# Performance work log

Hardware: AMD Instinct MI355X
Metric: run time of the kernel (lower is better)

## Reference

```python
import jax, jax.numpy as jnp
import numpy as np
from jax.ops import segment_sum, segment_max

N, D, B = 1536, 32, 8            # nodes, candidate out-degree per node, sequential batch steps
OBS, HID, HEADS, C = 33, 64, 4, 8  # obs_dim, GRU hidden, attn heads, out_dim//heads
E = N * D


def setup_inputs() -> dict:
    key = jax.random.key(0)
    ks = jax.random.split(key, 16)
    g = lambda i, shape, s=0.1: jax.random.normal(ks[i], shape, jnp.float32) * s
    src = jnp.repeat(jnp.arange(N), D)                    # uniform degree -> scatter_topk = row top-k
    dst = jax.random.randint(ks[0], (E,), 0, N)
    return dict(
        H_t=jax.random.normal(ks[1], (B, N, OBS), jnp.float32),
        src=src, dst=dst, k=4,
        W_e1=g(2, (OBS, 32)), b_e1=jnp.zeros(32), W_e2=g(3, (32, 32)), b_e2=jnp.zeros(32),
        ln_g=jnp.ones(32), ln_b=jnp.zeros(32),
        W_ih=g(4, (3 * HID, 32)), W_hh=g(5, (3 * HID, HID)),
        b_ih=jnp.zeros(3 * HID), b_hh=jnp.zeros(3 * HID),
        W_s1=g(6, (2 * HID, 64)), b_s1=jnp.zeros(64), W_s2=g(7, (64, 1)), b_s2=jnp.zeros(1),
        W_gat=g(8, (HID, HEADS * C)), att_src=g(9, (HEADS, C)), att_dst=g(10, (HEADS, C)),
        b_gat=jnp.zeros(HEADS * C),
    )


def _layernorm(x, g, b, eps=1e-5):
    mu = x.mean(-1, keepdims=True)
    var = ((x - mu) ** 2).mean(-1, keepdims=True)
    return (x - mu) * jax.lax.rsqrt(var + eps) * g + b


def _forward(H_t, src, dst, k, W_e1, b_e1, W_e2, b_e2, ln_g, ln_b,
             W_ih, W_hh, b_ih, b_hh, W_s1, b_s1, W_s2, b_s2,
             W_gat, att_src, att_dst, b_gat):
    # ObsEmbedding: Linear-ReLU-Linear-ReLU-LayerNorm, applied to all (B,N) at once
    x = jax.nn.relu(H_t @ W_e1 + b_e1)
    x = jax.nn.relu(x @ W_e2 + b_e2)
    H_emb = _layernorm(x, ln_g, ln_b)              # (B,N,32)

    def step(h, e_t):
        # --- NodeMemory: shared GRUCell, h carried across batch steps ---
        gi = e_t @ W_ih.T + b_ih                   # (N,3H)
        gh = h @ W_hh.T + b_hh
        i_r, i_z, i_n = jnp.split(gi, 3, -1)
        h_r, h_z, h_n = jnp.split(gh, 3, -1)
        r = jax.nn.sigmoid(i_r + h_r)
        z = jax.nn.sigmoid(i_z + h_z)
        n = jnp.tanh(i_n + r * h_n)
        h_new = (1.0 - z) * n + z * h              # (N,HID)

        # --- EdgeScorer: sigmoid MLP score per candidate edge, keep top-k per source ---
        feat = jnp.concatenate([h_new[src], h_new[dst]], -1)        # (E,2*HID)
        score = jax.nn.sigmoid(
            (jax.nn.relu(feat @ W_s1 + b_s1) @ W_s2 + b_s2)[:, 0])  # (E,)
        s2 = score.reshape(N, D)
        top_idx = jax.lax.top_k(s2, k)[1]                           # (N,k)
        keep = (jnp.zeros((N, D), bool)
                .at[jnp.arange(N)[:, None], top_idx].set(True)).reshape(-1)  # (E,)
        w = jnp.where(keep, score, 0.0)                             # soft edge weights

        # --- GATConv (add_self_loops=False), pruned edges masked out of the softmax ---
        xh = (h_new @ W_gat).reshape(N, HEADS, C)
        a_s = (xh * att_src).sum(-1)               # (N,HEADS)
        a_d = (xh * att_dst).sum(-1)
        logit = jax.nn.leaky_relu(a_s[src] + a_d[dst], 0.2)         # (E,HEADS)
        logit = jnp.where(keep[:, None], logit, -1e30)
        m = segment_max(logit, dst, num_segments=N)                 # softmax grouped by target
        ex = jnp.where(keep[:, None], jnp.exp(logit - m[dst]), 0.0)
        ssum = segment_sum(ex, dst, num_segments=N)
        alpha = ex / jnp.clip(ssum[dst], 1e-16)                     # (E,HEADS)

        msg = alpha[:, :, None] * xh[src] * w[:, None, None]        # edge_weight scales messages
        out = segment_sum(msg, dst, num_segments=N).reshape(N, HEADS * C) + b_gat

        # --- densify attention: scatter-accumulate then row-normalize ---
        A = jnp.zeros((HEADS, N, N), alpha.dtype).at[:, src, dst].add(alpha.T)
        A = A / jnp.clip(A.sum(-1, keepdims=True), 1e-9)
        return h_new, (out, A)

    h0 = jnp.zeros((N, HID), H_t.dtype)
    _, (outs, attns) = jax.lax.scan(step, h0, H_emb)
    return outs, attns                              # (B,N,32), (B,HEADS,N,N)


def reference(H_t, src, dst, k, W_e1, b_e1, W_e2, b_e2, ln_g, ln_b,
              W_ih, W_hh, b_ih, b_hh, W_s1, b_s1, W_s2, b_s2,
              W_gat, att_src, att_dst, b_gat):
    return _forward(H_t, src, dst, k, W_e1, b_e1, W_e2, b_e2, ln_g, ln_b,
                    W_ih, W_hh, b_ih, b_hh, W_s1, b_s1, W_s2, b_s2,
                    W_gat, att_src, att_dst, b_gat)
```

## Files before the change

### kernel.cpp

```cpp
#include <hip/hip_runtime.h>
#include <math.h>

#define NN   1536
#define DG   32
#define BB   8
#define OBSD 33
#define HID  64
#define NHEAD 4
#define EE   (NN*DG)

__device__ __forceinline__ float sigm(float x){ return 1.0f/(1.0f+expf(-x)); }

__global__ void __launch_bounds__(256) k_embgi(
                      const float* __restrict__ Ht,
                      const float* __restrict__ We1, const float* __restrict__ be1,
                      const float* __restrict__ We2, const float* __restrict__ be2,
                      const float* __restrict__ lng, const float* __restrict__ lnb,
                      const float* __restrict__ Wih, const float* __restrict__ bih,
                      float* __restrict__ GI, int* __restrict__ cursor){
    __shared__ float lwih[192*33];
    int tid = threadIdx.x;
    if(blockIdx.x < 6) cursor[blockIdx.x*256 + tid] = 0;
    for(int i=tid;i<192*32;i+=256){ int r=i>>5, c=i&31; lwih[r*33+c]=Wih[i]; }
    __syncthreads();
    int lane = tid & 63;
    int j32 = lane & 31;
    int bn = blockIdx.x*4 + (tid>>6);
    const float* hrow = Ht + (size_t)bn*OBSD;
    float x1 = be1[j32];
    for(int o=0;o<OBSD;o++) x1 += hrow[o]*We1[o*32+j32];
    x1 = fmaxf(x1,0.f);
    float x2 = be2[j32];
    for(int i=0;i<32;i++){
        float xi = __shfl(x1, (lane & 32) | i, 64);
        x2 += xi * We2[i*32+j32];
    }
    x2 = fmaxf(x2,0.f);
    float mu = x2;
    for(int m=16;m>=1;m>>=1) mu += __shfl_xor(mu, m, 32);
    mu *= (1.0f/32.0f);
    float d = x2-mu; float var = d*d;
    for(int m=16;m>=1;m>>=1) var += __shfl_xor(var, m, 32);
    var *= (1.0f/32.0f);
    float xln = d*rsqrtf(var+1e-5f)*lng[j32]+lnb[j32];
    int j = lane;
    float gr=bih[j], gz=bih[64+j], gn=bih[128+j];
    for(int kk=0;kk<32;kk++){
        float ek = __shfl(xln, kk, 64);
        gr += ek*lwih[j*33+kk];
        gz += ek*lwih[(64+j)*33+kk];
        gn += ek*lwih[(128+j)*33+kk];
    }
    float* g = GI + (size_t)bn*192;
    g[j]=gr; g[64+j]=gz; g[128+j]=gn;
}

__global__ void k_count(const int* __restrict__ dst, int* __restrict__ cursor){
    int e = blockIdx.x*256+threadIdx.x;
    if(e<EE) atomicAdd(&cursor[dst[e]],1);
}
__global__ void k_scan(int* __restrict__ cnt, int* __restrict__ indptr){
    __shared__ int part[256];
    int t = threadIdx.x;
    int local[6]; int s=0;
    for(int i=0;i<6;i++){ local[i]=cnt[t*6+i]; s+=local[i]; }
    part[t]=s; __syncthreads();
    if(t==0){ int acc=0; for(int i=0;i<256;i++){ int v=part[i]; part[i]=acc; acc+=v; } }
    __syncthreads();
    int pre = part[t];
    for(int i=0;i<6;i++){ int idx=t*6+i; indptr[idx]=pre; cnt[idx]=pre; pre+=local[i]; }
    if(t==255) indptr[NN]=EE;
}
__global__ void k_fill(const int* __restrict__ dst, int* __restrict__ cursor, int* __restrict__ eids){
    int e = blockIdx.x*256+threadIdx.x;
    if(e<EE){ int p = atomicAdd(&cursor[dst[e]],1); eids[p]=e; }
}

__global__ void __launch_bounds__(384) k_gru2(const float* __restrict__ GI,
                       const float* __restrict__ Whh, const float* __restrict__ bhh,
                       float* __restrict__ Hall){
    __shared__ float lw[192*65];
    __shared__ float hb[3][64];
    __shared__ float part[3][2][192];
    int tid = threadIdx.x;
    for(int i=tid;i<192*64;i+=384){ int r=i>>6, c=i&63; lw[r*65+c]=Whh[i]; }
    int wv = tid>>6;
    int nl = wv>>1;
    int half = wv&1;
    int j = tid&63;
    int node = blockIdx.x*3 + nl;
    if(half==0) hb[nl][j] = 0.f;
    __syncthreads();
    float b_r=bhh[j], b_z=bhh[64+j], b_n=bhh[128+j];
    const float* lwr = lw + j*65;
    const float* lwz = lw + (64+j)*65;
    const float* lwn = lw + (128+j)*65;
    int kb = half*32;
    for(int t=0;t<BB;t++){
        float hr=0.f, hz=0.f, hn=0.f;
        for(int kk=kb;kk<kb+32;kk++){
            float hk = hb[nl][kk];
            hr += hk*lwr[kk];
            hz += hk*lwz[kk];
            hn += hk*lwn[kk];
        }
        part[nl][half][j]     = hr;
        part[nl][half][64+j]  = hz;
        part[nl][half][128+j] = hn;
        __syncthreads();
        float hrT = part[nl][0][j]     + part[nl][1][j]     + b_r;
        float hzT = part[nl][0][64+j]  + part[nl][1][64+j]  + b_z;
        float hnT = part[nl][0][128+j] + part[nl][1][128+j] + b_n;
        const float* g = GI + ((size_t)t*NN+node)*192;
        float r  = sigm(g[j]     + hrT);
        float z  = sigm(g[64+j]  + hzT);
        float nn_= tanhf(g[128+j] + r*hnT);
        float hnew = (1.f-z)*nn_ + z*hb[nl][j];
        __syncthreads();
        if(half==0){
            hb[nl][j] = hnew;
            Hall[((size_t)t*NN+node)*64 + j] = hnew;
        }
        __syncthreads();
    }
}

__global__ void __launch_bounds__(256) k_post(const float* __restrict__ Hall,
                       const float* __restrict__ Ws1, const float* __restrict__ Wgat,
                       const float* __restrict__ atts, const float* __restrict__ attd,
                       float* __restrict__ P, float* __restrict__ Q,
                       float* __restrict__ xh, float* __restrict__ as_, float* __restrict__ ad_){
    __shared__ float ws1l[128*64];
    __shared__ float wgl[64*32];
    __shared__ float hb[4][64];
    int tid = threadIdx.x;
    for(int i=tid;i<128*64;i+=256) ws1l[i]=Ws1[i];
    for(int i=tid;i<64*32;i+=256)  wgl[i]=Wgat[i];
    __syncthreads();
    int nl = tid>>6;
    int bn = blockIdx.x*4 + nl;
    int j = tid&63;
    hb[nl][j] = Hall[(size_t)bn*64+j];
    float p=0.f,q=0.f,xv=0.f;
    for(int kk=0;kk<64;kk++){
        float hk = hb[nl][kk];
        p += hk*ws1l[kk*64+j];
        q += hk*ws1l[(64+kk)*64+j];
        if(j<32) xv += hk*wgl[kk*32+j];
    }
    P[(size_t)bn*64+j]=p; Q[(size_t)bn*64+j]=q;
    if(j<32){
        xh[(size_t)bn*32+j]=xv;
        float asv = xv*atts[j];
        float adv = xv*attd[j];
        for(int m=1;m<8;m<<=1){ asv += __shfl_xor(asv,m); adv += __shfl_xor(adv,m); }
        if((j&7)==0){ as_[(size_t)bn*4+(j>>3)]=asv; ad_[(size_t)bn*4+(j>>3)]=adv; }
    }
}

__global__ void __launch_bounds__(256) k_edge(const float* __restrict__ P, const float* __restrict__ Q,
                       const float* __restrict__ bs1, const float* __restrict__ Ws2,
                       const float* __restrict__ bs2, const int* __restrict__ dst,
                       const int* __restrict__ kptr, float* __restrict__ wbuf){
    int tid = threadIdx.x;
    int t = blockIdx.y;
    int row = blockIdx.x*8 + (tid>>5);
    int d = tid & 31;
    int e = row*DG + d;
    int de = dst[e];
    const float4* Pr = (const float4*)(P + ((size_t)t*NN+row)*64);
    const float4* Qr = (const float4*)(Q + ((size_t)t*NN+de)*64);
    const float4* B1 = (const float4*)bs1;
    const float4* W2 = (const float4*)Ws2;
    float acc = 0.f;
    #pragma unroll
    for(int jj=0;jj<16;jj++){
        float4 pv=Pr[jj], qv=Qr[jj], bv=B1[jj], wv=W2[jj];
        acc += fmaxf(pv.x+qv.x+bv.x,0.f)*wv.x;
        acc += fmaxf(pv.y+qv.y+bv.y,0.f)*wv.y;
        acc += fmaxf(pv.z+qv.z+bv.z,0.f)*wv.z;
        acc += fmaxf(pv.w+qv.w+bv.w,0.f)*wv.w;
    }
    float score = sigm(acc + bs2[0]);
    int kk = kptr[0]; if(kk>32) kk=32; if(kk<0) kk=0;
    bool sel=false;
    for(int it=0; it<kk; it++){
        float v = sel ? -INFINITY : score;
        int idx = d;
        for(int m=16;m>=1;m>>=1){
            float ov = __shfl_xor(v,m,32);
            int   oi = __shfl_xor(idx,m,32);
            if(ov>v || (ov==v && oi<idx)){ v=ov; idx=oi; }
        }
        if(idx==d) sel=true;
    }
    wbuf[(size_t)t*EE + e] = sel ? score : 0.f;
}

__global__ void __launch_bounds__(256) k_soft(const int* __restrict__ indptr, const int* __restrict__ eids,
                       const float* __restrict__ as_, const float* __restrict__ ad_,
                       const float* __restrict__ wbuf, const float* __restrict__ xhb,
                       const float* __restrict__ bgat,
                       float* __restrict__ alphab, float* __restrict__ outp){
    int n = blockIdx.x;
    int t = blockIdx.y;
    int h = threadIdx.x>>6;
    int lane = threadIdx.x&63;
    const float* w     = wbuf  + (size_t)t*EE;
    const float* asb   = as_   + (size_t)t*NN*4;
    const float* xhbt  = xhb   + (size_t)t*NN*32;
    float*       alpha = alphab+ (size_t)t*EE*4;
    int beg = indptr[n], end = indptr[n+1];
    int deg = end-beg;
    float adv = ad_[((size_t)t*NN+n)*4+h];
    float acc[8];
    #pragma unroll
    for(int c=0;c<8;c++) acc[c]=0.f;
    if(deg<=64){
        bool valid = lane<deg;
        int e = valid ? eids[beg+lane] : 0;
        float we = valid ? w[e] : 0.f;
        bool kept = we>0.f;
        int s = e>>5;
        float lg = -INFINITY, ex = 0.f;
        if(kept){
            lg = asb[s*4+h]+adv;
            lg = lg>0.f ? lg : 0.2f*lg;
        }
        float m = lg;
        for(int mm=32;mm>=1;mm>>=1) m = fmaxf(m,__shfl_xor(m,mm));
        if(kept) ex = expf(lg-m);
        float ssum = ex;
        for(int mm=32;mm>=1;mm>>=1) ssum += __shfl_xor(ssum,mm);
        float inv = 1.0f/fmaxf(ssum,1e-16f);
        if(kept){
            float a = ex*inv;
            alpha[e*4+h] = a;
            float aw = a*we;
            const float4* xr = (const float4*)(xhbt + s*32 + h*8);
            float4 x0 = xr[0], x1 = xr[1];
            acc[0]+=aw*x0.x; acc[1]+=aw*x0.y; acc[2]+=aw*x0.z; acc[3]+=aw*x0.w;
            acc[4]+=aw*x1.x; acc[5]+=aw*x1.y; acc[6]+=aw*x1.z; acc[7]+=aw*x1.w;
        }
    } else {
        float m = -INFINITY;
        for(int i=beg+lane;i<end;i+=64){
            int e = eids[i];
            if(w[e]>0.f){
                float lg = asb[(e>>5)*4+h]+adv;
                lg = lg>0.f ? lg : 0.2f*lg;
                m = fmaxf(m,lg);
            }
        }
        for(int mm=32;mm>=1;mm>>=1) m = fmaxf(m,__shfl_xor(m,mm));
        float ssum=0.f;
        for(int i=beg+lane;i<end;i+=64){
            int e = eids[i];
            float ex = 0.f;
            if(w[e]>0.f){
                float lg = asb[(e>>5)*4+h]+adv;
                lg = lg>0.f ? lg : 0.2f*lg;
                ex = expf(lg-m);
            }
            alpha[e*4+h]=ex;
            ssum += ex;
        }
        for(int mm=32;mm>=1;mm>>=1) ssum += __shfl_xor(ssum,mm);
        float inv = 1.0f/fmaxf(ssum,1e-16f);
        for(int i=beg+lane;i<end;i+=64){
            int e = eids[i];
            if(w[e]>0.f){
                float a = alpha[e*4+h]*inv;
                alpha[e*4+h]=a;
                float aw = a*w[e];
                const float* xr = xhbt + (e>>5)*32 + h*8;
                #pragma unroll
                for(int c=0;c<8;c++) acc[c] += aw*xr[c];
            }
        }
    }
    for(int mm=32;mm>=1;mm>>=1){
        #pragma unroll
        for(int c=0;c<8;c++) acc[c] += __shfl_xor(acc[c],mm);
    }
    if(lane==0){
        float* o = outp + ((size_t)t*NN+n)*32 + h*8;
        float4 o0 = { acc[0]+bgat[h*8+0], acc[1]+bgat[h*8+1], acc[2]+bgat[h*8+2], acc[3]+bgat[h*8+3] };
        float4 o1 = { acc[4]+bgat[h*8+4], acc[5]+bgat[h*8+5], acc[6]+bgat[h*8+6], acc[7]+bgat[h*8+7] };
        ((float4*)o)[0]=o0; ((float4*)o)[1]=o1;
    }
}

__global__ void __launch_bounds__(256) k_scatter(const float* __restrict__ alphab,
                       const float* __restrict__ wbuf,
                       const int* __restrict__ dst, float* __restrict__ attn){
    __shared__ int   kde[DG];
    __shared__ float kan[DG][NHEAD];
    __shared__ int   scnt;
    int n = blockIdx.x;
    int t = blockIdx.y;
    int tid = threadIdx.x;
    const float* alpha = alphab + (size_t)t*EE*4;
    const float* w     = wbuf   + (size_t)t*EE;
    if(tid<64){
        int d = tid;
        int e = n*DG + d;
        bool kept = false;
        if(d<DG) kept = (w[e] > 0.f);
        unsigned long long mask = __ballot(kept);
        float4 av = {0.f,0.f,0.f,0.f};
        int de = 0;
        if(kept){ de = dst[e]; av = *(const float4*)(alpha + (size_t)e*4); }
        float s0=av.x, s1=av.y, s2=av.z, s3=av.w;
        for(int m=32;m>=1;m>>=1){
            s0 += __shfl_xor(s0,m); s1 += __shfl_xor(s1,m);
            s2 += __shfl_xor(s2,m); s3 += __shfl_xor(s3,m);
        }
        if(kept){
            int pos = __popcll(mask & ((1ull<<d)-1ull));
            kde[pos] = de;
            kan[pos][0] = av.x / fmaxf(s0,1e-9f);
            kan[pos][1] = av.y / fmaxf(s1,1e-9f);
            kan[pos][2] = av.z / fmaxf(s2,1e-9f);
            kan[pos][3] = av.w / fmaxf(s3,1e-9f);
        }
        if(tid==0) scnt = __popcll(mask);
    }
    __syncthreads();
    int cnt = scnt;
    size_t base = (size_t)t*NHEAD*NN*NN + (size_t)n*NN;
    #pragma unroll
    for(int it=0; it<6; it++){
        int c = it*256 + tid;
        int h = c/(NN/4), c4 = c%(NN/4);
        float4 f4 = {0.f,0.f,0.f,0.f};
        for(int p=0;p<cnt;p++){
            int de = kde[p];
            if((de>>2)==c4) ((float*)&f4)[de&3] += kan[p][h];
        }
        ((float4*)(attn + base + (size_t)h*NN*NN))[c4] = f4;
    }
}

extern "C" void kernel_launch(void* const* d_in, const int* in_sizes, int n_in,
                              void* d_out, int out_size, void* d_ws, size_t ws_size,
                              hipStream_t stream) {
    const float* Ht   = (const float*)d_in[0];
    const int*   dst  = (const int*)  d_in[2];
    const int*   kptr = (const int*)  d_in[3];
    const float* We1  = (const float*)d_in[4];
    const float* be1  = (const float*)d_in[5];
    const float* We2  = (const float*)d_in[6];
    const float* be2  = (const float*)d_in[7];
    const float* lng  = (const float*)d_in[8];
    const float* lnb  = (const float*)d_in[9];
    const float* Wih  = (const float*)d_in[10];
    const float* Whh  = (const float*)d_in[11];
    const float* bih  = (const float*)d_in[12];
    const float* bhh  = (const float*)d_in[13];
    const float* Ws1  = (const float*)d_in[14];
    const float* bs1  = (const float*)d_in[15];
    const float* Ws2  = (const float*)d_in[16];
    const float* bs2  = (const float*)d_in[17];
    const float* Wgat = (const float*)d_in[18];
    const float* atts = (const float*)d_in[19];
    const float* attd = (const float*)d_in[20];
    const float* bgat = (const float*)d_in[21];

    float* outp = (float*)d_out;
    float* attn = outp + (size_t)BB*NN*32;

    float* ws    = (float*)d_ws;
    float* GI    = ws;
    float* Hall  = ws + 2359296;
    float* P     = ws + 3145728;
    float* Q     = ws + 3932160;
    float* xh    = ws + 4718592;
    float* as_   = ws + 5111808;
    float* ad_   = ws + 5160960;
    float* wbuf  = ws + 5210112;
    float* alpha = ws + 5603328;
    int*   ibase = (int*)(ws + 7176192);
    int*   cursor= ibase;
    int*   indptr= ibase + 2048;
    int*   eids  = ibase + 4096;

    k_embgi<<<BB*NN/4, 256, 0, stream>>>(Ht, We1, be1, We2, be2, lng, lnb, Wih, bih, GI, cursor);
    k_count<<<EE/256, 256, 0, stream>>>(dst, cursor);
    k_scan<<<1, 256, 0, stream>>>(cursor, indptr);
    k_fill<<<EE/256, 256, 0, stream>>>(dst, cursor, eids);
    k_gru2<<<NN/3, 384, 0, stream>>>(GI, Whh, bhh, Hall);
    k_post<<<BB*NN/4, 256, 0, stream>>>(Hall, Ws1, Wgat, atts, attd, P, Q, xh, as_, ad_);
    {
        dim3 ge(NN/8, BB);
        k_edge<<<ge, 256, 0, stream>>>(P, Q, bs1, Ws2, bs2, dst, kptr, wbuf);
        dim3 g(NN, BB);
        k_soft<<<g, 256, 0, stream>>>(indptr, eids, as_, ad_, wbuf, xh, bgat, alpha, outp);
        k_scatter<<<g, 256, 0, stream>>>(alpha, wbuf, dst, attn);
    }
}
```

Measured before the change: 537.9 us.

## Fuse CSR build into one block kernel and cache GRU weights in registers

Merges the count, scan and fill kernels into a single 1024-thread block that builds the destination CSR using shared-memory atomics, which removes two kernel launches and global atomics. The cost is that a single block now processes all 49K edges serially on one CU. Separately, the GRU kernel preloads each thread's 96 recurrent weights into registers and unrolls the dot product, so the per-step loop no longer reads weights from LDS. This raises register pressure, and the launch bound is set to 3 blocks per CU.

```diff
diff --git a/kernel.cpp b/kernel.cpp
--- a/kernel.cpp
+++ b/kernel.cpp
@@ -17,10 +17,9 @@
                       const float* __restrict__ We2, const float* __restrict__ be2,
                       const float* __restrict__ lng, const float* __restrict__ lnb,
                       const float* __restrict__ Wih, const float* __restrict__ bih,
-                      float* __restrict__ GI, int* __restrict__ cursor){
+                      float* __restrict__ GI){
     __shared__ float lwih[192*33];
     int tid = threadIdx.x;
-    if(blockIdx.x < 6) cursor[blockIdx.x*256 + tid] = 0;
     for(int i=tid;i<192*32;i+=256){ int r=i>>5, c=i&31; lwih[r*33+c]=Wih[i]; }
     __syncthreads();
     int lane = tid & 63;
@@ -55,28 +54,33 @@
     g[j]=gr; g[64+j]=gz; g[128+j]=gn;
 }
 
-__global__ void k_count(const int* __restrict__ dst, int* __restrict__ cursor){
-    int e = blockIdx.x*256+threadIdx.x;
-    if(e<EE) atomicAdd(&cursor[dst[e]],1);
-}
-__global__ void k_scan(int* __restrict__ cnt, int* __restrict__ indptr){
+__global__ void __launch_bounds__(1024) k_csr(const int* __restrict__ dst,
+                                              int* __restrict__ indptr, int* __restrict__ eids){
+    __shared__ int cnt[NN];
     __shared__ int part[256];
-    int t = threadIdx.x;
+    int tid = threadIdx.x;
+    for(int i=tid;i<NN;i+=1024) cnt[i]=0;
+    __syncthreads();
+    for(int e=tid;e<EE;e+=1024) atomicAdd(&cnt[dst[e]],1);
+    __syncthreads();
     int local[6]; int s=0;
-    for(int i=0;i<6;i++){ local[i]=cnt[t*6+i]; s+=local[i]; }
-    part[t]=s; __syncthreads();
-    if(t==0){ int acc=0; for(int i=0;i<256;i++){ int v=part[i]; part[i]=acc; acc+=v; } }
-    __syncthreads();
-    int pre = part[t];
-    for(int i=0;i<6;i++){ int idx=t*6+i; indptr[idx]=pre; cnt[idx]=pre; pre+=local[i]; }
-    if(t==255) indptr[NN]=EE;
-}
-__global__ void k_fill(const int* __restrict__ dst, int* __restrict__ cursor, int* __restrict__ eids){
-    int e = blockIdx.x*256+threadIdx.x;
-    if(e<EE){ int p = atomicAdd(&cursor[dst[e]],1); eids[p]=e; }
-}
-
-__global__ void __launch_bounds__(384) k_gru2(const float* __restrict__ GI,
+    if(tid<256){
+        for(int i=0;i<6;i++){ local[i]=cnt[tid*6+i]; s+=local[i]; }
+        part[tid]=s;
+    }
+    __syncthreads();
+    if(tid==0){ int acc=0; for(int i=0;i<256;i++){ int v=part[i]; part[i]=acc; acc+=v; } }
+    __syncthreads();
+    if(tid<256){
+        int pre = part[tid];
+        for(int i=0;i<6;i++){ int idx=tid*6+i; indptr[idx]=pre; cnt[idx]=pre; pre+=local[i]; }
+        if(tid==255) indptr[NN]=EE;
+    }
+    __syncthreads();
+    for(int e=tid;e<EE;e+=1024){ int p = atomicAdd(&cnt[dst[e]],1); eids[p]=e; }
+}
+
+__global__ void __launch_bounds__(384,3) k_gru3(const float* __restrict__ GI,
                        const float* __restrict__ Whh, const float* __restrict__ bhh,
                        float* __restrict__ Hall){
     __shared__ float lw[192*65];
@@ -91,18 +95,23 @@
     int node = blockIdx.x*3 + nl;
     if(half==0) hb[nl][j] = 0.f;
     __syncthreads();
+    int kb = half*32;
+    float rw[32], rz[32], rn[32];
+    #pragma unroll
+    for(int i=0;i<32;i++){
+        rw[i]=lw[j*65+kb+i];
+        rz[i]=lw[(64+j)*65+kb+i];
+        rn[i]=lw[(128+j)*65+kb+i];
+    }
     float b_r=bhh[j], b_z=bhh[64+j], b_n=bhh[128+j];
-    const float* lwr = lw + j*65;
-    const float* lwz = lw + (64+j)*65;
-    const float* lwn = lw + (128+j)*65;
-    int kb = half*32;
     for(int t=0;t<BB;t++){
         float hr=0.f, hz=0.f, hn=0.f;
-        for(int kk=kb;kk<kb+32;kk++){
-            float hk = hb[nl][kk];
-            hr += hk*lwr[kk];
-            hz += hk*lwz[kk];
-            hn += hk*lwn[kk];
+        #pragma unroll
+        for(int i=0;i<32;i++){
+            float hk = hb[nl][kb+i];
+            hr += hk*rw[i];
+            hz += hk*rz[i];
+            hn += hk*rn[i];
         }
         part[nl][half][j]     = hr;
         part[nl][half][64+j]  = hz;
@@ -381,15 +390,12 @@
     float* wbuf  = ws + 5210112;
     float* alpha = ws + 5603328;
     int*   ibase = (int*)(ws + 7176192);
-    int*   cursor= ibase;
-    int*   indptr= ibase + 2048;
-    int*   eids  = ibase + 4096;
-
-    k_embgi<<<BB*NN/4, 256, 0, stream>>>(Ht, We1, be1, We2, be2, lng, lnb, Wih, bih, GI, cursor);
-    k_count<<<EE/256, 256, 0, stream>>>(dst, cursor);
-    k_scan<<<1, 256, 0, stream>>>(cursor, indptr);
-    k_fill<<<EE/256, 256, 0, stream>>>(dst, cursor, eids);
-    k_gru2<<<NN/3, 384, 0, stream>>>(GI, Whh, bhh, Hall);
+    int*   indptr= ibase;
+    int*   eids  = ibase + 2048;
+
+    k_embgi<<<BB*NN/4, 256, 0, stream>>>(Ht, We1, be1, We2, be2, lng, lnb, Wih, bih, GI);
+    k_csr<<<1, 1024, 0, stream>>>(dst, indptr, eids);
+    k_gru3<<<NN/3, 384, 0, stream>>>(GI, Whh, bhh, Hall);
     k_post<<<BB*NN/4, 256, 0, stream>>>(Hall, Ws1, Wgat, atts, attd, P, Q, xh, as_, ad_);
     {
         dim3 ge(NN/8, BB);
```

New measurement: 558.1 us. 3.8% more time.
